# Kernel tuning notes

Measured on AMD Instinct MI355X. Metric: run time of the kernel, lower is better.

Reference implementation:

```python
import jax, jax.numpy as jnp
import numpy as np

B, N, HID = 8, 512, 512
HEADS, HD = 16, 32
FFN, DEMB = 2048, 64
EPS = 1e-5


def layer_norm(x, g, b):
    mu = jnp.mean(x, axis=-1, keepdims=True)
    var = jnp.var(x, axis=-1, keepdims=True)
    return (x - mu) * jax.lax.rsqrt(var + EPS) * g + b


def setup_inputs() -> dict:
    key = jax.random.key(0)
    ks = jax.random.split(key, 16)
    s = lambda fan_in: 1.0 / np.sqrt(fan_in)
    return {
        "x": jax.random.normal(ks[0], (B, N, HID), jnp.float32),
        "distance_features": jax.random.normal(ks[1], (B, N, N, DEMB), jnp.float32),
        "edge_mask": jax.random.randint(ks[2], (B, N, N), 0, 2) > 0,
        "qkv_w": jax.random.uniform(ks[3], (HID, 3 * HID), jnp.float32, -s(HID), s(HID)),
        "qkv_b": jnp.zeros((3 * HID,), jnp.float32),
        "out_w": jax.random.uniform(ks[4], (HID, HID), jnp.float32, -s(HID), s(HID)),
        "out_b": jnp.zeros((HID,), jnp.float32),
        "dist_w": jax.random.uniform(ks[5], (DEMB, HEADS), jnp.float32, -s(DEMB), s(DEMB)),
        "dist_b": jnp.zeros((HEADS,), jnp.float32),
        "ln1_g": jnp.ones((HID,), jnp.float32),
        "ln1_b": jnp.zeros((HID,), jnp.float32),
        "ln2_g": jnp.ones((HID,), jnp.float32),
        "ln2_b": jnp.zeros((HID,), jnp.float32),
        "ff1_w": jax.random.uniform(ks[6], (HID, FFN), jnp.float32, -s(HID), s(HID)),
        "ff1_b": jnp.zeros((FFN,), jnp.float32),
        "ff2_w": jax.random.uniform(ks[7], (FFN, HID), jnp.float32, -s(FFN), s(FFN)),
        "ff2_b": jnp.zeros((HID,), jnp.float32),
    }


def reference(x, distance_features, edge_mask, qkv_w, qkv_b, out_w, out_b,
              dist_w, dist_b, ln1_g, ln1_b, ln2_g, ln2_b,
              ff1_w, ff1_b, ff2_w, ff2_b):
    residual = x
    h = layer_norm(x, ln1_g, ln1_b)
    qkv = h @ qkv_w + qkv_b  # [B,N,3*HID]
    q, k, v = jnp.split(qkv, 3, axis=-1)
    q = q.reshape(B, N, HEADS, HD)
    k = k.reshape(B, N, HEADS, HD)
    v = v.reshape(B, N, HEADS, HD)
    scale = jnp.sqrt(jnp.float32(HD))
    scores = jnp.einsum('bihd,bjhd->bhij', q, k) / scale  # [B,H,N,N]
    bias = distance_features @ dist_w + dist_b  # [B,N,N,H]
    scores = scores + jnp.transpose(bias, (0, 3, 1, 2))
    neg = jnp.finfo(scores.dtype).min
    scores = jnp.where(edge_mask[:, None, :, :], scores, neg)
    attn = jax.nn.softmax(scores, axis=-1)
    ctx = jnp.einsum('bhij,bjhd->bihd', attn, v).reshape(B, N, HID)
    x = residual + ctx @ out_w + out_b
    y = layer_norm(x, ln2_g, ln2_b)
    ff = jax.nn.gelu(y @ ff1_w + ff1_b, approximate=False) @ ff2_w + ff2_b
    return x + ff
```

## Files before the change

kernel.cpp:

```cpp
#include <hip/hip_runtime.h>
#include <cstddef>
#include <cstdint>

#define B_     8
#define N_     512
#define HID_   512
#define HEADS_ 16
#define HD_    32
#define FFN_   2048
#define DEMB_  64
#define ROWS   (B_*N_)

typedef unsigned short u16;
typedef short bf16x8 __attribute__((ext_vector_type(8)));
typedef float f32x4  __attribute__((ext_vector_type(4)));
typedef short short8v __attribute__((ext_vector_type(8)));

__device__ __forceinline__ u16 f2bf(float f) {
  unsigned u = __float_as_uint(f);
  u += 0x7fffu + ((u >> 16) & 1u);
  return (u16)(u >> 16);
}

__device__ __forceinline__ void gload16(const void* g, void* l) {
  __builtin_amdgcn_global_load_lds(
      (const __attribute__((address_space(1))) unsigned int*)g,
      (__attribute__((address_space(3))) unsigned int*)l, 16, 0, 0);
}

__global__ void detect_mask_kernel(const unsigned char* __restrict__ m,
                                   int* __restrict__ flag) {
  int t = blockIdx.x * blockDim.x + threadIdx.x;
  if ((t & 3) != 0) {
    if (m[t] != 0) atomicOr(flag, 1);
  }
}

__global__ __launch_bounds__(256) void ln_kernel(const float* __restrict__ x,
                                                 const float* __restrict__ g,
                                                 const float* __restrict__ bt,
                                                 u16* __restrict__ y) {
  const int lane = threadIdx.x & 63;
  const int row  = blockIdx.x * 4 + (threadIdx.x >> 6);
  const float* xr = x + (size_t)row * HID_;
  float4 v0 = *(const float4*)(xr + lane * 8);
  float4 v1 = *(const float4*)(xr + lane * 8 + 4);
  float s = v0.x + v0.y + v0.z + v0.w + v1.x + v1.y + v1.z + v1.w;
  float q = v0.x*v0.x + v0.y*v0.y + v0.z*v0.z + v0.w*v0.w
          + v1.x*v1.x + v1.y*v1.y + v1.z*v1.z + v1.w*v1.w;
  #pragma unroll
  for (int off = 32; off > 0; off >>= 1) {
    s += __shfl_xor(s, off, 64);
    q += __shfl_xor(q, off, 64);
  }
  const float mean = s * (1.0f / HID_);
  const float var  = q * (1.0f / HID_) - mean * mean;
  const float rs   = rsqrtf(var + 1e-5f);
  const float4 g0 = *(const float4*)(g + lane * 8);
  const float4 g1 = *(const float4*)(g + lane * 8 + 4);
  const float4 b0 = *(const float4*)(bt + lane * 8);
  const float4 b1 = *(const float4*)(bt + lane * 8 + 4);
  short8v o;
  o[0] = (short)f2bf((v0.x - mean) * rs * g0.x + b0.x);
  o[1] = (short)f2bf((v0.y - mean) * rs * g0.y + b0.y);
  o[2] = (short)f2bf((v0.z - mean) * rs * g0.z + b0.z);
  o[3] = (short)f2bf((v0.w - mean) * rs * g0.w + b0.w);
  o[4] = (short)f2bf((v1.x - mean) * rs * g1.x + b1.x);
  o[5] = (short)f2bf((v1.y - mean) * rs * g1.y + b1.y);
  o[6] = (short)f2bf((v1.z - mean) * rs * g1.z + b1.z);
  o[7] = (short)f2bf((v1.w - mean) * rs * g1.w + b1.w);
  *(short8v*)(y + (size_t)row * HID_ + lane * 8) = o;
}

__global__ __launch_bounds__(256) void wt_kernel(const float* __restrict__ W,
                                                 u16* __restrict__ Wt,
                                                 int K, int N) {
  __shared__ float tile[32][33];
  const int t = threadIdx.x;
  const int n0 = blockIdx.x * 32, k0 = blockIdx.y * 32;
  const int tx = t & 31, ty = t >> 5;
  #pragma unroll
  for (int i = 0; i < 4; ++i)
    tile[ty + 8 * i][tx] = W[(size_t)(k0 + ty + 8 * i) * N + n0 + tx];
  __syncthreads();
  #pragma unroll
  for (int i = 0; i < 4; ++i) {
    const int n = ty + 8 * i;
    Wt[(size_t)(n0 + n) * K + k0 + tx] = f2bf(tile[tx][n]);
  }
}

template <int ACT, bool HAS_RES, bool OUT_BF16>
__global__ __launch_bounds__(256) void mfma_gemm(
    const u16* __restrict__ A, const u16* __restrict__ Wt,
    const float* __restrict__ bias, const float* __restrict__ res,
    void* __restrict__ Cout, int N, int K) {
  __shared__ __align__(16) u16 As[128 * 64];
  __shared__ __align__(16) u16 Bs[128 * 64];
  const int t    = threadIdx.x;
  const int wid  = t >> 6, lane = t & 63;
  const int wr   = wid >> 1, wc = wid & 1;
  const int m0   = blockIdx.y * 128, n0 = blockIdx.x * 128;
  const int srow8 = lane >> 3;
  const int sslot = (lane & 7) ^ srow8;

  f32x4 zero = {0.f, 0.f, 0.f, 0.f};
  f32x4 acc[4][4];
  #pragma unroll
  for (int m = 0; m < 4; ++m)
    #pragma unroll
    for (int n = 0; n < 4; ++n) acc[m][n] = zero;

  for (int kt = 0; kt < K; kt += 64) {
    __syncthreads();
    #pragma unroll
    for (int i = 0; i < 4; ++i) {
      const int rbase = wid * 32 + i * 8;
      const int r = rbase + srow8;
      gload16(A  + (size_t)(m0 + r) * K + kt + sslot * 8, &As[rbase * 64]);
      gload16(Wt + (size_t)(n0 + r) * K + kt + sslot * 8, &Bs[rbase * 64]);
    }
    __syncthreads();
    #pragma unroll
    for (int kk = 0; kk < 2; ++kk) {
      bf16x8 a[4], b[4];
      #pragma unroll
      for (int m = 0; m < 4; ++m) {
        const int row = wr * 64 + m * 16 + (lane & 15);
        const int s   = (kk * 4 + (lane >> 4)) ^ (row & 7);
        a[m] = *(const bf16x8*)&As[row * 64 + s * 8];
      }
      #pragma unroll
      for (int n = 0; n < 4; ++n) {
        const int row = wc * 64 + n * 16 + (lane & 15);
        const int s   = (kk * 4 + (lane >> 4)) ^ (row & 7);
        b[n] = *(const bf16x8*)&Bs[row * 64 + s * 8];
      }
      #pragma unroll
      for (int m = 0; m < 4; ++m)
        #pragma unroll
        for (int n = 0; n < 4; ++n)
          acc[m][n] = __builtin_amdgcn_mfma_f32_16x16x32_bf16(
              a[m], b[n], acc[m][n], 0, 0, 0);
    }
  }
  #pragma unroll
  for (int n = 0; n < 4; ++n) {
    const int col = n0 + wc * 64 + n * 16 + (lane & 15);
    const float bb = bias[col];
    #pragma unroll
    for (int m = 0; m < 4; ++m) {
      #pragma unroll
      for (int j = 0; j < 4; ++j) {
        const int row = m0 + wr * 64 + m * 16 + (lane >> 4) * 4 + j;
        float v = acc[m][n][j] + bb;
        if (ACT == 1) v = 0.5f * v * (1.0f + erff(v * 0.70710678118654752f));
        const size_t off = (size_t)row * N + col;
        if (HAS_RES) v += res[off];
        if (OUT_BF16) ((u16*)Cout)[off] = f2bf(v);
        else          ((float*)Cout)[off] = v;
      }
    }
  }
}

__global__ __launch_bounds__(256) void bias_kernel(
    const float* __restrict__ df, const unsigned char* __restrict__ mask8,
    const float* __restrict__ dw, const float* __restrict__ db,
    const int* __restrict__ flag, float* __restrict__ biasb) {
  __shared__ float dfs[128][68];
  const int t    = threadIdx.x;
  const int tile = blockIdx.x & 3;
  const int i    = (blockIdx.x >> 2) & 511;
  const int b    = blockIdx.x >> 11;
  const int j0   = tile * 128;
  const int h    = t >> 4;
  const int jt   = t & 15;

  const float4* gsrc =
      (const float4*)(df + (((size_t)b * N_ + i) * N_ + j0) * DEMB_);
  #pragma unroll
  for (int s = 0; s < 8; ++s) {
    const int f   = s * 256 + t;
    const int row = f >> 4, d4 = f & 15;
    *(float4*)&dfs[row][d4 * 4] = gsrc[f];
  }

  float4 w[16];
  #pragma unroll
  for (int d4 = 0; d4 < 16; ++d4) {
    w[d4].x = dw[(d4 * 4 + 0) * HEADS_ + h];
    w[d4].y = dw[(d4 * 4 + 1) * HEADS_ + h];
    w[d4].z = dw[(d4 * 4 + 2) * HEADS_ + h];
    w[d4].w = dw[(d4 * 4 + 3) * HEADS_ + h];
  }
  const float bh = db[h];
  const int fb = *flag;
  const int* mask32 = (const int*)mask8;
  const size_t mbase = ((size_t)b * N_ + i) * N_ + j0;
  float* obase = biasb + (((size_t)b * HEADS_ + h) * N_ + i) * N_ + j0;
  __syncthreads();

  for (int s = 0; s < 8; ++s) {
    const int jl = s * 16 + jt;
    float a0 = 0.f, a1 = 0.f, a2 = 0.f, a3 = 0.f;
    #pragma unroll
    for (int d4 = 0; d4 < 16; ++d4) {
      const float4 v = *(const float4*)&dfs[jl][d4 * 4];
      a0 += v.x * w[d4].x;
      a1 += v.y * w[d4].y;
      a2 += v.z * w[d4].z;
      a3 += v.w * w[d4].w;
    }
    const float acc = (a0 + a1) + (a2 + a3) + bh;
    const bool mv = fb ? (mask8[mbase + jl] != 0) : (mask32[mbase + jl] != 0);
    obase[jl] = mv ? acc : -1e30f;
  }
}

__global__ __launch_bounds__(256) void attn_kernel(
    const float* __restrict__ qkv, const float* __restrict__ biasb,
    u16* __restrict__ ctx) {
  __shared__ float Ks[N_][HD_];
  __shared__ float Vs[N_][HD_];
  const int t    = threadIdx.x;
  const int b    = blockIdx.x >> 5;
  const int hh   = (blockIdx.x >> 1) & 15;
  const int half = blockIdx.x & 1;
  const size_t qbase = (size_t)b * N_ * (3 * HID_);
  for (int idx = t; idx < N_ * 8; idx += 256) {
    const int j = idx >> 3, f = idx & 7;
    const float* kp = qkv + qbase + (size_t)j * (3 * HID_) + HID_ + hh * HD_ + f * 4;
    *(float4*)&Ks[j][f * 4] = *(const float4*)kp;
    *(float4*)&Vs[j][f * 4] = *(const float4*)(kp + HID_);
  }
  __syncthreads();
  const int i = half * 256 + t;
  const float* qp = qkv + qbase + (size_t)i * (3 * HID_) + hh * HD_;
  float q[HD_];
  #pragma unroll
  for (int f = 0; f < 8; ++f) {
    const float4 v = *(const float4*)(qp + f * 4);
    q[f * 4 + 0] = v.x; q[f * 4 + 1] = v.y; q[f * 4 + 2] = v.z; q[f * 4 + 3] = v.w;
  }
  const float* brow = biasb + (((size_t)b * HEADS_ + hh) * N_ + i) * N_;
  float m = -3.0e38f, l = 0.f;
  float o[HD_];
  #pragma unroll
  for (int d = 0; d < HD_; ++d) o[d] = 0.f;
  for (int j4 = 0; j4 < N_; j4 += 4) {
    const float4 bq = *(const float4*)(brow + j4);
    const float bbv[4] = {bq.x, bq.y, bq.z, bq.w};
    #pragma unroll
    for (int c = 0; c < 4; ++c) {
      const int j = j4 + c;
      float s0 = 0.f, s1 = 0.f, s2 = 0.f, s3 = 0.f;
      #pragma unroll
      for (int d = 0; d < HD_; d += 4) {
        s0 += q[d + 0] * Ks[j][d + 0];
        s1 += q[d + 1] * Ks[j][d + 1];
        s2 += q[d + 2] * Ks[j][d + 2];
        s3 += q[d + 3] * Ks[j][d + 3];
      }
      float s = (s0 + s1) + (s2 + s3);
      s = s * 0.17677669529663687f + bbv[c];
      if (s > m) {
        const float corr = __expf(m - s);
        l *= corr;
        #pragma unroll
        for (int d = 0; d < HD_; ++d) o[d] *= corr;
        m = s;
      }
      const float p = __expf(s - m);
      l += p;
      #pragma unroll
      for (int d = 0; d < HD_; ++d) o[d] += p * Vs[j][d];
    }
  }
  const float inv = 1.0f / l;
  u16* cp = ctx + (((size_t)b * N_ + i) * HEADS_ + hh) * HD_;
  #pragma unroll
  for (int f = 0; f < 4; ++f) {
    short8v v;
    #pragma unroll
    for (int e = 0; e < 8; ++e) v[e] = (short)f2bf(o[f * 8 + e] * inv);
    *(short8v*)(cp + f * 8) = v;
  }
}

extern "C" void kernel_launch(void* const* d_in, const int* in_sizes, int n_in,
                              void* d_out, int out_size, void* d_ws, size_t ws_size,
                              hipStream_t stream) {
  const float* x      = (const float*)d_in[0];
  const float* df     = (const float*)d_in[1];
  const unsigned char* mask = (const unsigned char*)d_in[2];
  const float* qkv_w  = (const float*)d_in[3];
  const float* qkv_b  = (const float*)d_in[4];
  const float* out_w  = (const float*)d_in[5];
  const float* out_b  = (const float*)d_in[6];
  const float* dist_w = (const float*)d_in[7];
  const float* dist_b = (const float*)d_in[8];
  const float* ln1_g  = (const float*)d_in[9];
  const float* ln1_b  = (const float*)d_in[10];
  const float* ln2_g  = (const float*)d_in[11];
  const float* ln2_b  = (const float*)d_in[12];
  const float* ff1_w  = (const float*)d_in[13];
  const float* ff1_b  = (const float*)d_in[14];
  const float* ff2_w  = (const float*)d_in[15];
  const float* ff2_b  = (const float*)d_in[16];
  float* out = (float*)d_out;

  char* p = (char*)d_ws;
  auto alloc = [&](size_t bytes) {
    char* r = p;
    p += (bytes + 255) & ~(size_t)255;
    return r;
  };
  float* qkv    = (float*)alloc((size_t)ROWS * 3 * HID_ * 4);
  float* biasb  = (float*)alloc((size_t)B_ * HEADS_ * N_ * N_ * 4);
  float* xa     = (float*)alloc((size_t)ROWS * HID_ * 4);
  u16*   h16    = (u16*)alloc((size_t)ROWS * HID_ * 2);
  u16*   ctx16  = (u16*)alloc((size_t)ROWS * HID_ * 2);
  u16*   y16    = (u16*)alloc((size_t)ROWS * HID_ * 2);
  u16*   ff116  = (u16*)alloc((size_t)ROWS * FFN_ * 2);
  u16*   qkv_wt = (u16*)alloc((size_t)3 * HID_ * HID_ * 2);
  u16*   out_wt = (u16*)alloc((size_t)HID_ * HID_ * 2);
  u16*   ff1_wt = (u16*)alloc((size_t)FFN_ * HID_ * 2);
  u16*   ff2_wt = (u16*)alloc((size_t)HID_ * FFN_ * 2);
  int*   flag   = (int*)alloc(sizeof(int));

  hipMemsetAsync(flag, 0, sizeof(int), stream);
  detect_mask_kernel<<<256, 256, 0, stream>>>(mask, flag);

  wt_kernel<<<dim3(3 * HID_ / 32, HID_ / 32), 256, 0, stream>>>(qkv_w, qkv_wt, HID_, 3 * HID_);
  wt_kernel<<<dim3(HID_ / 32, HID_ / 32), 256, 0, stream>>>(out_w, out_wt, HID_, HID_);
  wt_kernel<<<dim3(FFN_ / 32, HID_ / 32), 256, 0, stream>>>(ff1_w, ff1_wt, HID_, FFN_);
  wt_kernel<<<dim3(HID_ / 32, FFN_ / 32), 256, 0, stream>>>(ff2_w, ff2_wt, FFN_, HID_);

  ln_kernel<<<ROWS / 4, 256, 0, stream>>>(x, ln1_g, ln1_b, h16);
  mfma_gemm<0, false, false><<<dim3(3 * HID_ / 128, ROWS / 128), 256, 0, stream>>>(
      h16, qkv_wt, qkv_b, nullptr, qkv, 3 * HID_, HID_);
  bias_kernel<<<B_ * N_ * 4, 256, 0, stream>>>(df, mask, dist_w, dist_b, flag, biasb);
  attn_kernel<<<B_ * HEADS_ * 2, 256, 0, stream>>>(qkv, biasb, ctx16);
  mfma_gemm<0, true, false><<<dim3(HID_ / 128, ROWS / 128), 256, 0, stream>>>(
      ctx16, out_wt, out_b, x, xa, HID_, HID_);
  ln_kernel<<<ROWS / 4, 256, 0, stream>>>(xa, ln2_g, ln2_b, y16);
  mfma_gemm<1, false, true><<<dim3(FFN_ / 128, ROWS / 128), 256, 0, stream>>>(
      y16, ff1_wt, ff1_b, nullptr, ff116, FFN_, HID_);
  mfma_gemm<0, true, false><<<dim3(HID_ / 128, ROWS / 128), 256, 0, stream>>>(
      ff116, ff2_wt, ff2_b, xa, out, HID_, FFN_);
}
```

Baseline: 538.8 us.

## Split attention over key quarters, store bias and K as bf16

The attention kernel now launches four times as many blocks. Each block handles 64 query rows, and its four waves each process a quarter of the keys. The partial softmax states (m, l, o) are merged through shared memory at the end. The bias buffer is stored as bf16, halving its write and read traffic. K is staged in LDS as bf16, V is read directly from global memory with wave-uniform addresses, and the running-max rescale is skipped unless the new score exceeds the max by more than 8. These changes aim to fix low occupancy and heavy bias bandwidth, at the cost of reduced precision in the bias and K and an extra merge step.

```diff
diff --git a/kernel.cpp b/kernel.cpp
--- a/kernel.cpp
+++ b/kernel.cpp
@@ -15,11 +15,15 @@
 typedef short bf16x8 __attribute__((ext_vector_type(8)));
 typedef float f32x4  __attribute__((ext_vector_type(4)));
 typedef short short8v __attribute__((ext_vector_type(8)));
+typedef short short4v __attribute__((ext_vector_type(4)));
 
 __device__ __forceinline__ u16 f2bf(float f) {
   unsigned u = __float_as_uint(f);
   u += 0x7fffu + ((u >> 16) & 1u);
   return (u16)(u >> 16);
+}
+__device__ __forceinline__ float bf2f(u16 b) {
+  return __uint_as_float(((unsigned)b) << 16);
 }
 
 __device__ __forceinline__ void gload16(const void* g, void* l) {
@@ -167,7 +171,7 @@
 __global__ __launch_bounds__(256) void bias_kernel(
     const float* __restrict__ df, const unsigned char* __restrict__ mask8,
     const float* __restrict__ dw, const float* __restrict__ db,
-    const int* __restrict__ flag, float* __restrict__ biasb) {
+    const int* __restrict__ flag, u16* __restrict__ biasb) {
   __shared__ float dfs[128][68];
   const int t    = threadIdx.x;
   const int tile = blockIdx.x & 3;
@@ -198,7 +202,7 @@
   const int fb = *flag;
   const int* mask32 = (const int*)mask8;
   const size_t mbase = ((size_t)b * N_ + i) * N_ + j0;
-  float* obase = biasb + (((size_t)b * HEADS_ + h) * N_ + i) * N_ + j0;
+  u16* obase = biasb + (((size_t)b * HEADS_ + h) * N_ + i) * N_ + j0;
   __syncthreads();
 
   for (int s = 0; s < 8; ++s) {
@@ -214,57 +218,77 @@
     }
     const float acc = (a0 + a1) + (a2 + a3) + bh;
     const bool mv = fb ? (mask8[mbase + jl] != 0) : (mask32[mbase + jl] != 0);
-    obase[jl] = mv ? acc : -1e30f;
+    obase[jl] = f2bf(mv ? acc : -1e30f);
   }
 }
 
 __global__ __launch_bounds__(256) void attn_kernel(
-    const float* __restrict__ qkv, const float* __restrict__ biasb,
+    const float* __restrict__ qkv, const u16* __restrict__ biasb,
     u16* __restrict__ ctx) {
-  __shared__ float Ks[N_][HD_];
-  __shared__ float Vs[N_][HD_];
+  __shared__ union {
+    u16 k[N_ * HD_];
+    struct {
+      float po[3][64][33];
+      float pm[3][64];
+      float pl[3][64];
+    } c;
+  } sm;
   const int t    = threadIdx.x;
-  const int b    = blockIdx.x >> 5;
-  const int hh   = (blockIdx.x >> 1) & 15;
-  const int half = blockIdx.x & 1;
+  const int bx   = blockIdx.x;
+  const int b    = bx >> 7;
+  const int h    = (bx >> 3) & 15;
+  const int iblk = bx & 7;
+  const int jq   = t >> 6;
+  const int r    = t & 63;
+  const int i    = iblk * 64 + r;
   const size_t qbase = (size_t)b * N_ * (3 * HID_);
+
   for (int idx = t; idx < N_ * 8; idx += 256) {
     const int j = idx >> 3, f = idx & 7;
-    const float* kp = qkv + qbase + (size_t)j * (3 * HID_) + HID_ + hh * HD_ + f * 4;
-    *(float4*)&Ks[j][f * 4] = *(const float4*)kp;
-    *(float4*)&Vs[j][f * 4] = *(const float4*)(kp + HID_);
+    const float4 kv = *(const float4*)(qkv + qbase + (size_t)j * (3 * HID_) +
+                                       HID_ + h * HD_ + f * 4);
+    short4v ks;
+    ks[0] = (short)f2bf(kv.x); ks[1] = (short)f2bf(kv.y);
+    ks[2] = (short)f2bf(kv.z); ks[3] = (short)f2bf(kv.w);
+    *(short4v*)&sm.k[j * HD_ + f * 4] = ks;
   }
   __syncthreads();
-  const int i = half * 256 + t;
-  const float* qp = qkv + qbase + (size_t)i * (3 * HID_) + hh * HD_;
+
   float q[HD_];
-  #pragma unroll
-  for (int f = 0; f < 8; ++f) {
-    const float4 v = *(const float4*)(qp + f * 4);
-    q[f * 4 + 0] = v.x; q[f * 4 + 1] = v.y; q[f * 4 + 2] = v.z; q[f * 4 + 3] = v.w;
-  }
-  const float* brow = biasb + (((size_t)b * HEADS_ + hh) * N_ + i) * N_;
+  {
+    const float* qp = qkv + qbase + (size_t)i * (3 * HID_) + h * HD_;
+    #pragma unroll
+    for (int f = 0; f < 8; ++f) {
+      const float4 v = *(const float4*)(qp + f * 4);
+      q[f*4+0] = v.x * 0.17677669529663687f;
+      q[f*4+1] = v.y * 0.17677669529663687f;
+      q[f*4+2] = v.z * 0.17677669529663687f;
+      q[f*4+3] = v.w * 0.17677669529663687f;
+    }
+  }
+  const u16* brow = biasb + (((size_t)b * HEADS_ + h) * N_ + i) * N_ + jq * 128;
+  const float* vbase = qkv + qbase + 2 * HID_ + h * HD_;
   float m = -3.0e38f, l = 0.f;
   float o[HD_];
   #pragma unroll
   for (int d = 0; d < HD_; ++d) o[d] = 0.f;
-  for (int j4 = 0; j4 < N_; j4 += 4) {
-    const float4 bq = *(const float4*)(brow + j4);
-    const float bbv[4] = {bq.x, bq.y, bq.z, bq.w};
-    #pragma unroll
-    for (int c = 0; c < 4; ++c) {
-      const int j = j4 + c;
-      float s0 = 0.f, s1 = 0.f, s2 = 0.f, s3 = 0.f;
-      #pragma unroll
-      for (int d = 0; d < HD_; d += 4) {
-        s0 += q[d + 0] * Ks[j][d + 0];
-        s1 += q[d + 1] * Ks[j][d + 1];
-        s2 += q[d + 2] * Ks[j][d + 2];
-        s3 += q[d + 3] * Ks[j][d + 3];
-      }
-      float s = (s0 + s1) + (s2 + s3);
-      s = s * 0.17677669529663687f + bbv[c];
-      if (s > m) {
+
+  for (int j8 = 0; j8 < 128; j8 += 8) {
+    const short8v bq = *(const short8v*)(brow + j8);
+    #pragma unroll
+    for (int e = 0; e < 8; ++e) {
+      const int j = jq * 128 + j8 + e;
+      const u16* kr = &sm.k[j * HD_];
+      float s = 0.f;
+      #pragma unroll
+      for (int c = 0; c < 4; ++c) {
+        const short8v kk = *(const short8v*)(kr + c * 8);
+        #pragma unroll
+        for (int d = 0; d < 8; ++d)
+          s += q[c*8+d] * bf2f((u16)kk[d]);
+      }
+      s += bf2f((u16)bq[e]);
+      if (s - m > 8.0f) {
         const float corr = __expf(m - s);
         l *= corr;
         #pragma unroll
@@ -273,18 +297,45 @@
       }
       const float p = __expf(s - m);
       l += p;
-      #pragma unroll
-      for (int d = 0; d < HD_; ++d) o[d] += p * Vs[j][d];
-    }
-  }
-  const float inv = 1.0f / l;
-  u16* cp = ctx + (((size_t)b * N_ + i) * HEADS_ + hh) * HD_;
-  #pragma unroll
-  for (int f = 0; f < 4; ++f) {
-    short8v v;
-    #pragma unroll
-    for (int e = 0; e < 8; ++e) v[e] = (short)f2bf(o[f * 8 + e] * inv);
-    *(short8v*)(cp + f * 8) = v;
+      const float4* vr = (const float4*)(vbase + (size_t)j * (3 * HID_));
+      #pragma unroll
+      for (int c = 0; c < 8; ++c) {
+        const float4 vv = vr[c];
+        o[c*4+0] += p * vv.x; o[c*4+1] += p * vv.y;
+        o[c*4+2] += p * vv.z; o[c*4+3] += p * vv.w;
+      }
+    }
+  }
+
+  __syncthreads();
+  if (jq > 0) {
+    sm.c.pm[jq-1][r] = m;
+    sm.c.pl[jq-1][r] = l;
+    #pragma unroll
+    for (int d = 0; d < HD_; ++d) sm.c.po[jq-1][r][d] = o[d];
+  }
+  __syncthreads();
+  if (jq == 0) {
+    #pragma unroll
+    for (int p2 = 0; p2 < 3; ++p2) {
+      const float m2 = sm.c.pm[p2][r], l2 = sm.c.pl[p2][r];
+      const float mn = fmaxf(m, m2);
+      const float c1 = __expf(m - mn), c2 = __expf(m2 - mn);
+      l = l * c1 + l2 * c2;
+      #pragma unroll
+      for (int d = 0; d < HD_; ++d)
+        o[d] = o[d] * c1 + sm.c.po[p2][r][d] * c2;
+      m = mn;
+    }
+    const float inv = 1.0f / l;
+    u16* cp = ctx + (((size_t)b * N_ + i) * HEADS_ + h) * HD_;
+    #pragma unroll
+    for (int f = 0; f < 4; ++f) {
+      short8v v;
+      #pragma unroll
+      for (int e = 0; e < 8; ++e) v[e] = (short)f2bf(o[f*8+e] * inv);
+      *(short8v*)(cp + f * 8) = v;
+    }
   }
 }
 
@@ -317,7 +368,7 @@
     return r;
   };
   float* qkv    = (float*)alloc((size_t)ROWS * 3 * HID_ * 4);
-  float* biasb  = (float*)alloc((size_t)B_ * HEADS_ * N_ * N_ * 4);
+  u16*   biasb  = (u16*)alloc((size_t)B_ * HEADS_ * N_ * N_ * 2);
   float* xa     = (float*)alloc((size_t)ROWS * HID_ * 4);
   u16*   h16    = (u16*)alloc((size_t)ROWS * HID_ * 2);
   u16*   ctx16  = (u16*)alloc((size_t)ROWS * HID_ * 2);
@@ -341,7 +392,7 @@
   mfma_gemm<0, false, false><<<dim3(3 * HID_ / 128, ROWS / 128), 256, 0, stream>>>(
       h16, qkv_wt, qkv_b, nullptr, qkv, 3 * HID_, HID_);
   bias_kernel<<<B_ * N_ * 4, 256, 0, stream>>>(df, mask, dist_w, dist_b, flag, biasb);
-  attn_kernel<<<B_ * HEADS_ * 2, 256, 0, stream>>>(qkv, biasb, ctx16);
+  attn_kernel<<<B_ * HEADS_ * 8, 256, 0, stream>>>(qkv, biasb, ctx16);
   mfma_gemm<0, true, false><<<dim3(HID_ / 128, ROWS / 128), 256, 0, stream>>>(
       ctx16, out_wt, out_b, x, xa, HID_, HID_);
   ln_kernel<<<ROWS / 4, 256, 0, stream>>>(xa, ln2_g, ln2_b, y16);
```

Result: no change. 529.8 us (-1.7%).
